# Optimization experiments

Measured on AMD Instinct MI355X. Metric: run time of the kernel, lower is better.

Reference implementation:

```python
import jax, jax.numpy as jnp
import numpy as np
from jax import lax

B, T, H, THETA_DIM = 64, 2048, 256, 5
L1, L2, OUT = 256, 256, 1


def _p(key, shape, fan_in):
    return jax.random.normal(key, shape, dtype=jnp.float32) / np.sqrt(fan_in)


def setup_inputs() -> dict:
    key = jax.random.key(0)
    ks = jax.random.split(key, 16)
    inp = {
        "x": jax.random.normal(ks[0], (B, T), dtype=jnp.float32),
        "theta": jax.random.normal(ks[1], (B, THETA_DIM), dtype=jnp.float32),
        # LSTM layer 0 (input dim 1): gate order [i, f, g, o]
        "Wx0": _p(ks[2], (1, 4 * H), 1),
        "Wh0": _p(ks[3], (H, 4 * H), H),
        "b0": jnp.zeros((4 * H,), dtype=jnp.float32),
        # LSTM layer 1 (input dim H)
        "Wx1": _p(ks[4], (H, 4 * H), H),
        "Wh1": _p(ks[5], (H, 4 * H), H),
        "b1": jnp.zeros((4 * H,), dtype=jnp.float32),
        # theta projector Dense(H)
        "Wtp": _p(ks[6], (THETA_DIM, H), THETA_DIM),
        "btp": jnp.zeros((H,), dtype=jnp.float32),
        # MLP head: concat(H + H) -> 256 -> 256 -> 1
        "Wl1": _p(ks[7], (2 * H, L1), 2 * H),
        "bl1": jnp.zeros((L1,), dtype=jnp.float32),
        "Wl2": _p(ks[8], (L1, L2), L1),
        "bl2": jnp.zeros((L2,), dtype=jnp.float32),
        "Wo": _p(ks[9], (L2, OUT), L2),
        "bo": jnp.zeros((OUT,), dtype=jnp.float32),
    }
    return inp


def _lstm_layer(x_seq, Wx, Wh, b):
    # x_seq: [B, T, D]. Precompute input-to-gate GEMM once (big, batched),
    # leaving only the small recurrent matmul inside the scan.
    xg = jnp.einsum('btd,dg->btg', x_seq, Wx) + b  # [B, T, 4H]
    bsz = x_seq.shape[0]
    h = Wh.shape[0]
    c0 = jnp.zeros((bsz, h), dtype=x_seq.dtype)
    h0 = jnp.zeros((bsz, h), dtype=x_seq.dtype)

    def step(carry, xg_t):
        c, hh = carry
        gates = xg_t + hh @ Wh  # [B, 4H]
        i, f, g, o = jnp.split(gates, 4, axis=-1)
        c = jax.nn.sigmoid(f) * c + jax.nn.sigmoid(i) * jnp.tanh(g)
        hh = jax.nn.sigmoid(o) * jnp.tanh(c)
        return (c, hh), hh

    _, hs = lax.scan(step, (c0, h0), jnp.swapaxes(xg, 0, 1))  # hs: [T, B, H]
    return jnp.swapaxes(hs, 0, 1)  # [B, T, H]


def reference(x, theta, Wx0, Wh0, b0, Wx1, Wh1, b1, Wtp, btp,
              Wl1, bl1, Wl2, bl2, Wo, bo):
    h = x[:, :, None]  # [B, T, 1] (module expands 2-D input)
    h = _lstm_layer(h, Wx0, Wh0, b0)
    h = _lstm_layer(h, Wx1, Wh1, b1)
    h = jnp.mean(h, axis=1)  # mean_aggregation=True -> [B, H]
    tproj = theta @ Wtp + btp  # [B, H]
    z = jnp.concatenate([h, tproj], axis=-1)  # [B, 2H]
    z = jax.nn.elu(z @ Wl1 + bl1)
    z = jax.nn.elu(z @ Wl2 + bl2)
    return z @ Wo + bo  # [B, 1]
```

## Files before the change

kernel.cpp:

```cpp
#include <hip/hip_runtime.h>
#include <hip/hip_bf16.h>


#define BB 64
#define TT 2048
#define HH 256

typedef short s16x8 __attribute__((ext_vector_type(8)));
typedef float f32x4 __attribute__((ext_vector_type(4)));

__device__ inline unsigned short f2bf(float f) {
  unsigned u = __float_as_uint(f);
  u += 0x7fff + ((u >> 16) & 1);
  return (unsigned short)(u >> 16);
}
__device__ inline float sigm(float x) { return 1.f / (1.f + __expf(-x)); }
__device__ inline float tanh_f(float x) { return 1.f - 2.f / (__expf(2.f * x) + 1.f); }

__device__ inline void st_wt32(unsigned int* p, unsigned int v) {
  __hip_atomic_store(p, v, __ATOMIC_RELAXED, __HIP_MEMORY_SCOPE_AGENT);
}
__device__ inline void st_flag(int* p, int v) {
  __hip_atomic_store(p, v, __ATOMIC_RELAXED, __HIP_MEMORY_SCOPE_AGENT);
}
__device__ inline unsigned long long ld_wt64(const unsigned long long* p) {
  return __hip_atomic_load(p, __ATOMIC_RELAXED, __HIP_MEMORY_SCOPE_AGENT);
}
__device__ inline void wait_ge(const int* p, int tgt) {
  while (__hip_atomic_load(p, __ATOMIC_RELAXED, __HIP_MEMORY_SCOPE_AGENT) < tgt)
    __builtin_amdgcn_s_sleep(1);
}
__device__ inline s16x8 ld_frag_wt(const unsigned short* p) {
  union { unsigned long long q[2]; s16x8 v; } u;
  u.q[0] = ld_wt64((const unsigned long long*)p);
  u.q[1] = ld_wt64((const unsigned long long*)(p + 4));
  return u.v;
}

#define MFMA(a, b, c) __builtin_amdgcn_mfma_f32_16x16x32_bf16((a), (b), (c), 0, 0, 0)

__global__ void xt_kernel(const float* __restrict__ x, float* __restrict__ xT) {
  int i = blockIdx.x * 256 + threadIdx.x;
  int b = i & 63, t = i >> 6;
  xT[(size_t)t * BB + b] = x[(size_t)b * TT + t];
}

__global__ __launch_bounds__(256, 2)
void lstm_kernel(const float* __restrict__ Wx0, const float* __restrict__ Wh0,
                 const float* __restrict__ b0v,
                 const float* __restrict__ Wx1, const float* __restrict__ Wh1,
                 const float* __restrict__ b1v,
                 const float* __restrict__ xT,
                 unsigned short* __restrict__ seq0, unsigned short* __restrict__ ring,
                 float* __restrict__ hmean, int* flags)
{
  __shared__ float gbuf[2][16][4][33];

  const int tid  = threadIdx.x;
  const int lane = tid & 63;
  const int w    = tid >> 6;
  const int u16  = lane & 15;
  const int kgrp = lane >> 4;
  const int arow = lane & 15;
  const int gp   = w & 1;

  int* f0 = flags;
  int* f1 = flags + 512;

  const int bid = blockIdx.x;

  if (bid < 32) {
    const int g = bid >> 3, wg = bid & 7;
    const int b0r = g * 16;
    const int uh = w >> 1;
    const int ubase = wg * 32;
    s16x8 bw[16];
#pragma unroll
    for (int f = 0; f < 16; ++f) {
      const int nt = f >> 3, ks = f & 7;
      const int col = (2 * gp + nt) * 256 + ubase + uh * 16 + u16;
#pragma unroll
      for (int j = 0; j < 8; ++j)
        bw[f][j] = (short)f2bf(Wh0[(size_t)(ks * 32 + kgrp * 8 + j) * 1024 + col]);
    }
    const int eur = tid >> 4;
    const int eu2 = (tid & 15) * 2;
    float bE[2][4], xE[2][4];
#pragma unroll
    for (int uu = 0; uu < 2; ++uu)
#pragma unroll
      for (int ga = 0; ga < 4; ++ga) {
        const int col = ga * 256 + ubase + eu2 + uu;
        bE[uu][ga] = b0v[col];
        xE[uu][ga] = Wx0[col];
      }
    int* myflag = &f0[(g * 8 + wg) * 16];
    float cst[2] = {0.f, 0.f};

    for (int t = 0; t < TT; ++t) {
      if (t > 0 && tid < 8) wait_ge(&f0[(g * 8 + tid) * 16], t);
      __syncthreads();

      f32x4 acc0 = {0, 0, 0, 0}, acc1 = {0, 0, 0, 0};
      if (t > 0) {
        const unsigned short* sp = seq0 + ((size_t)(t - 1) * BB + b0r + arow) * HH;
        s16x8 a[8];
#pragma unroll
        for (int ks = 0; ks < 8; ++ks) a[ks] = *(const s16x8*)(sp + ks * 32 + kgrp * 8);
#pragma unroll
        for (int ks = 0; ks < 8; ++ks) {
          acc0 = MFMA(a[ks], bw[ks], acc0);
          acc1 = MFMA(a[ks], bw[8 + ks], acc1);
        }
      }
#pragma unroll
      for (int r = 0; r < 4; ++r) {
        gbuf[0][kgrp * 4 + r][2 * gp + 0][uh * 16 + u16] = acc0[r];
        gbuf[0][kgrp * 4 + r][2 * gp + 1][uh * 16 + u16] = acc1[r];
      }
      __syncthreads();

      const float xval = xT[(size_t)t * BB + b0r + eur];
      unsigned short hb[2];
#pragma unroll
      for (int uu = 0; uu < 2; ++uu) {
        const int ul = eu2 + uu;
        const float gi = gbuf[0][eur][0][ul] + bE[uu][0] + xval * xE[uu][0];
        const float gf = gbuf[0][eur][1][ul] + bE[uu][1] + xval * xE[uu][1];
        const float gg = gbuf[0][eur][2][ul] + bE[uu][2] + xval * xE[uu][2];
        const float go = gbuf[0][eur][3][ul] + bE[uu][3] + xval * xE[uu][3];
        cst[uu] = sigm(gf) * cst[uu] + sigm(gi) * tanh_f(gg);
        const float hv = sigm(go) * tanh_f(cst[uu]);
        hb[uu] = f2bf(hv);
      }
      st_wt32((unsigned int*)(seq0 + ((size_t)t * BB + b0r + eur) * HH + ubase + eu2),
              (unsigned int)hb[0] | ((unsigned int)hb[1] << 16));
      __syncthreads();
      if (tid == 0) st_flag(myflag, t + 1);
    }
  } else {
    const int idx = bid - 32;
    const int g = idx >> 4, q = idx & 15;
    const int b0r = g * 16;
    const int kh = w >> 1;
    s16x8 bw[16];
#pragma unroll
    for (int f = 0; f < 16; ++f) {
      const int nt = f >> 3, ks = f & 7;
      const int col = (2 * gp + nt) * 256 + q * 16 + u16;
#pragma unroll
      for (int j = 0; j < 8; ++j) {
        const int k = ks * 32 + kgrp * 8 + j;
        const float wv = (kh == 0) ? Wx1[(size_t)k * 1024 + col]
                                   : Wh1[(size_t)k * 1024 + col];
        bw[f][j] = (short)f2bf(wv);
      }
    }
    const int eur = tid >> 3;
    const int eu2 = (tid & 7) * 2;
    float bE[2][4];
#pragma unroll
    for (int uu = 0; uu < 2; ++uu)
#pragma unroll
      for (int ga = 0; ga < 4; ++ga)
        bE[uu][ga] = b1v[ga * 256 + q * 16 + eu2 + uu];
    int* myflag = &f1[(g * 16 + q) * 16];
    float cst[2] = {0.f, 0.f}, hs2[2] = {0.f, 0.f};

    for (int t = 0; t < TT; ++t) {
      if (tid < 8) wait_ge(&f0[(g * 8 + tid) * 16], t + 1);
      else if (t > 0 && tid < 24) wait_ge(&f1[(g * 16 + tid - 8) * 16], t);
      __syncthreads();

      f32x4 acc0 = {0, 0, 0, 0}, acc1 = {0, 0, 0, 0};
      if (kh == 0) {
        const unsigned short* sp = seq0 + ((size_t)t * BB + b0r + arow) * HH;
        s16x8 a[8];
#pragma unroll
        for (int ks = 0; ks < 8; ++ks) a[ks] = *(const s16x8*)(sp + ks * 32 + kgrp * 8);
#pragma unroll
        for (int ks = 0; ks < 8; ++ks) {
          acc0 = MFMA(a[ks], bw[ks], acc0);
          acc1 = MFMA(a[ks], bw[8 + ks], acc1);
        }
      } else if (t > 0) {
        const unsigned short* rp = ring + ((size_t)((t - 1) & 1) * BB + b0r + arow) * HH;
        s16x8 a[8];
#pragma unroll
        for (int ks = 0; ks < 8; ++ks) a[ks] = ld_frag_wt(rp + ks * 32 + kgrp * 8);
#pragma unroll
        for (int ks = 0; ks < 8; ++ks) {
          acc0 = MFMA(a[ks], bw[ks], acc0);
          acc1 = MFMA(a[ks], bw[8 + ks], acc1);
        }
      }
#pragma unroll
      for (int r = 0; r < 4; ++r) {
        gbuf[kh][kgrp * 4 + r][2 * gp + 0][u16] = acc0[r];
        gbuf[kh][kgrp * 4 + r][2 * gp + 1][u16] = acc1[r];
      }
      __syncthreads();

      if (tid < 128) {
        unsigned short hb[2];
#pragma unroll
        for (int uu = 0; uu < 2; ++uu) {
          const int ul = eu2 + uu;
          const float gi = gbuf[0][eur][0][ul] + gbuf[1][eur][0][ul] + bE[uu][0];
          const float gf = gbuf[0][eur][1][ul] + gbuf[1][eur][1][ul] + bE[uu][1];
          const float gg = gbuf[0][eur][2][ul] + gbuf[1][eur][2][ul] + bE[uu][2];
          const float go = gbuf[0][eur][3][ul] + gbuf[1][eur][3][ul] + bE[uu][3];
          cst[uu] = sigm(gf) * cst[uu] + sigm(gi) * tanh_f(gg);
          const float hv = sigm(go) * tanh_f(cst[uu]);
          hs2[uu] += hv;
          hb[uu] = f2bf(hv);
        }
        st_wt32((unsigned int*)(ring + ((size_t)(t & 1) * BB + b0r + eur) * HH + q * 16 + eu2),
                (unsigned int)hb[0] | ((unsigned int)hb[1] << 16));
      }
      __syncthreads();
      if (tid == 0) st_flag(myflag, t + 1);
    }
    if (tid < 128) {
#pragma unroll
      for (int uu = 0; uu < 2; ++uu)
        hmean[(size_t)(b0r + eur) * HH + q * 16 + eu2 + uu] = hs2[uu] * (1.f / TT);
    }
  }
}

__global__ __launch_bounds__(256)
void mlp_kernel(const float* __restrict__ theta, const float* __restrict__ Wtp,
                const float* __restrict__ btp, const float* __restrict__ Wl1,
                const float* __restrict__ bl1, const float* __restrict__ Wl2,
                const float* __restrict__ bl2, const float* __restrict__ Wo,
                const float* __restrict__ bo, const float* __restrict__ hmean,
                float* __restrict__ out)
{
  const int b = blockIdx.x;
  const int j = threadIdx.x;
  __shared__ float z[2 * HH];
  __shared__ float z1s[HH];
  __shared__ float red[256];

  float tp = btp[j];
#pragma unroll
  for (int d = 0; d < 5; ++d) tp += theta[b * 5 + d] * Wtp[d * HH + j];
  z[j] = hmean[(size_t)b * HH + j];
  z[HH + j] = tp;
  __syncthreads();

  float a1 = bl1[j];
  for (int k = 0; k < 2 * HH; ++k) a1 += z[k] * Wl1[(size_t)k * 256 + j];
  a1 = (a1 > 0.f) ? a1 : (__expf(a1) - 1.f);
  z1s[j] = a1;
  __syncthreads();

  float a2 = bl2[j];
  for (int k = 0; k < HH; ++k) a2 += z1s[k] * Wl2[(size_t)k * 256 + j];
  a2 = (a2 > 0.f) ? a2 : (__expf(a2) - 1.f);
  red[j] = a2 * Wo[j];
  __syncthreads();
  for (int s = 128; s > 0; s >>= 1) {
    if (j < s) red[j] += red[j + s];
    __syncthreads();
  }
  if (j == 0) out[b] = red[0] + bo[0];
}

extern "C" void kernel_launch(void* const* d_in, const int* in_sizes, int n_in,
                              void* d_out, int out_size, void* d_ws, size_t ws_size,
                              hipStream_t stream) {
  const float* x    = (const float*)d_in[0];
  const float* theta= (const float*)d_in[1];
  const float* Wx0  = (const float*)d_in[2];
  const float* Wh0  = (const float*)d_in[3];
  const float* b0   = (const float*)d_in[4];
  const float* Wx1  = (const float*)d_in[5];
  const float* Wh1  = (const float*)d_in[6];
  const float* b1   = (const float*)d_in[7];
  const float* Wtp  = (const float*)d_in[8];
  const float* btp  = (const float*)d_in[9];
  const float* Wl1  = (const float*)d_in[10];
  const float* bl1  = (const float*)d_in[11];
  const float* Wl2  = (const float*)d_in[12];
  const float* bl2  = (const float*)d_in[13];
  const float* Wo   = (const float*)d_in[14];
  const float* bo   = (const float*)d_in[15];

  char* ws = (char*)d_ws;
  int* flags           = (int*)ws;
  unsigned short* ring = (unsigned short*)(ws + 8192);
  float* hmean         = (float*)(ws + 8192 + 65536);
  float* xT            = (float*)(ws + 8192 + 65536 + 65536);
  unsigned short* seq0 = (unsigned short*)(ws + 8192 + 65536 + 65536 + 524288);
  const size_t WS_NEED = 8192ull + 65536 + 65536 + 524288 + (size_t)TT * BB * HH * 2ull;
  if (ws_size < WS_NEED) return;

  hipMemsetAsync(d_ws, 0, 8192, stream);

  xt_kernel<<<dim3((BB * TT) / 256), dim3(256), 0, stream>>>(x, xT);
  lstm_kernel<<<dim3(96), dim3(256), 0, stream>>>(
      Wx0, Wh0, b0, Wx1, Wh1, b1, xT, seq0, ring, hmean, flags);
  mlp_kernel<<<dim3(BB), dim3(256), 0, stream>>>(
      theta, Wtp, btp, Wl1, bl1, Wl2, bl2, Wo, bo, hmean, (float*)d_out);
}
```

Before: 6.681 ms.

## Repartition LSTM recurrence into 32 wider 512-thread blocks with fewer inter-block flags

Reduces the persistent LSTM kernel from 96 blocks of 256 threads to 32 blocks of 512 threads. Each block now owns 64 hidden units, so each batch group synchronises with 4 peer blocks per step instead of 8 or 16. Layer-1 blocks hold both Wx1 and Wh1 fragments per thread. They stage the previous hidden state through a swizzled LDS tile using wide atomic loads, and layer-0 flags are polled lazily via a cached 'seen' value. This cuts cross-block flag traffic and per-step sync latency, at the cost of more registers per thread and serial input-then-recurrent MFMA chains within a block.

```diff
diff --git a/kernel.cpp b/kernel.cpp
--- a/kernel.cpp
+++ b/kernel.cpp
@@ -17,24 +17,21 @@
 __device__ inline float sigm(float x) { return 1.f / (1.f + __expf(-x)); }
 __device__ inline float tanh_f(float x) { return 1.f - 2.f / (__expf(2.f * x) + 1.f); }
 
-__device__ inline void st_wt32(unsigned int* p, unsigned int v) {
+__device__ inline void st32(unsigned int* p, unsigned int v) {
   __hip_atomic_store(p, v, __ATOMIC_RELAXED, __HIP_MEMORY_SCOPE_AGENT);
 }
-__device__ inline void st_flag(int* p, int v) {
+__device__ inline void st32i(int* p, int v) {
   __hip_atomic_store(p, v, __ATOMIC_RELAXED, __HIP_MEMORY_SCOPE_AGENT);
 }
-__device__ inline unsigned long long ld_wt64(const unsigned long long* p) {
+__device__ inline int ld32i(const int* p) {
   return __hip_atomic_load(p, __ATOMIC_RELAXED, __HIP_MEMORY_SCOPE_AGENT);
 }
+__device__ inline unsigned long long ld64(const unsigned int* p) {
+  return __hip_atomic_load((const unsigned long long*)p, __ATOMIC_RELAXED,
+                           __HIP_MEMORY_SCOPE_AGENT);
+}
 __device__ inline void wait_ge(const int* p, int tgt) {
-  while (__hip_atomic_load(p, __ATOMIC_RELAXED, __HIP_MEMORY_SCOPE_AGENT) < tgt)
-    __builtin_amdgcn_s_sleep(1);
-}
-__device__ inline s16x8 ld_frag_wt(const unsigned short* p) {
-  union { unsigned long long q[2]; s16x8 v; } u;
-  u.q[0] = ld_wt64((const unsigned long long*)p);
-  u.q[1] = ld_wt64((const unsigned long long*)(p + 4));
-  return u.v;
+  while (ld32i(p) < tgt) __builtin_amdgcn_s_sleep(1);
 }
 
 #define MFMA(a, b, c) __builtin_amdgcn_mfma_f32_16x16x32_bf16((a), (b), (c), 0, 0, 0)
@@ -45,16 +42,18 @@
   xT[(size_t)t * BB + b] = x[(size_t)b * TT + t];
 }
 
-__global__ __launch_bounds__(256, 2)
+__global__ __launch_bounds__(512, 1)
 void lstm_kernel(const float* __restrict__ Wx0, const float* __restrict__ Wh0,
                  const float* __restrict__ b0v,
                  const float* __restrict__ Wx1, const float* __restrict__ Wh1,
                  const float* __restrict__ b1v,
                  const float* __restrict__ xT,
-                 unsigned short* __restrict__ seq0, unsigned short* __restrict__ ring,
+                 unsigned int* __restrict__ seq0,
+                 unsigned int* __restrict__ h1ring,
                  float* __restrict__ hmean, int* flags)
 {
-  __shared__ float gbuf[2][16][4][33];
+  __shared__ float gbuf[16][4][66];
+  __shared__ __align__(16) char Ab1[8192];
 
   const int tid  = threadIdx.x;
   const int lane = tid & 63;
@@ -62,170 +61,182 @@
   const int u16  = lane & 15;
   const int kgrp = lane >> 4;
   const int arow = lane & 15;
-  const int gp   = w & 1;
+  const int bid  = blockIdx.x;
 
   int* f0 = flags;
-  int* f1 = flags + 512;
-
-  const int bid = blockIdx.x;
-
-  if (bid < 32) {
-    const int g = bid >> 3, wg = bid & 7;
-    const int b0r = g * 16;
-    const int uh = w >> 1;
-    const int ubase = wg * 32;
-    s16x8 bw[16];
-#pragma unroll
-    for (int f = 0; f < 16; ++f) {
-      const int nt = f >> 3, ks = f & 7;
-      const int col = (2 * gp + nt) * 256 + ubase + uh * 16 + u16;
-#pragma unroll
-      for (int j = 0; j < 8; ++j)
-        bw[f][j] = (short)f2bf(Wh0[(size_t)(ks * 32 + kgrp * 8 + j) * 1024 + col]);
-    }
-    const int eur = tid >> 4;
-    const int eu2 = (tid & 15) * 2;
-    float bE[2][4], xE[2][4];
-#pragma unroll
-    for (int uu = 0; uu < 2; ++uu)
-#pragma unroll
-      for (int ga = 0; ga < 4; ++ga) {
-        const int col = ga * 256 + ubase + eu2 + uu;
-        bE[uu][ga] = b0v[col];
-        xE[uu][ga] = Wx0[col];
-      }
-    int* myflag = &f0[(g * 8 + wg) * 16];
-    float cst[2] = {0.f, 0.f};
+  int* f1 = flags + 256;
+
+  const int gp = w >> 2;
+  const int uo = (w & 3) * 16;
+  const int eur = tid >> 5;
+  const int eu2 = (tid & 31) * 2;
+
+  if (bid < 16) {
+    const int g = bid >> 2, wg = bid & 3;
+    const int ub = wg * 64;
+    s16x8 bw[2][8];
+#pragma unroll
+    for (int nt = 0; nt < 2; ++nt)
+#pragma unroll
+      for (int ks = 0; ks < 8; ++ks) {
+        const int col = (2 * gp + nt) * 256 + ub + uo + u16;
+#pragma unroll
+        for (int j = 0; j < 8; ++j)
+          bw[nt][ks][j] = (short)f2bf(Wh0[(size_t)(ks * 32 + kgrp * 8 + j) * 1024 + col]);
+      }
+    float bE[4][2], xE[4][2];
+#pragma unroll
+    for (int ga = 0; ga < 4; ++ga)
+#pragma unroll
+      for (int uu = 0; uu < 2; ++uu) {
+        const int c = ga * 256 + ub + eu2 + uu;
+        bE[ga][uu] = b0v[c]; xE[ga][uu] = Wx0[c];
+      }
+    int* myf = &f0[(g * 4 + wg) * 16];
+    float cL[2] = {0.f, 0.f};
 
     for (int t = 0; t < TT; ++t) {
-      if (t > 0 && tid < 8) wait_ge(&f0[(g * 8 + tid) * 16], t);
-      __syncthreads();
-
-      f32x4 acc0 = {0, 0, 0, 0}, acc1 = {0, 0, 0, 0};
+      if (t > 0 && tid < 4) wait_ge(&f0[(g * 4 + tid) * 16], t);
+      __syncthreads();
+
+      f32x4 acc0 = {0,0,0,0}, acc1 = {0,0,0,0};
       if (t > 0) {
-        const unsigned short* sp = seq0 + ((size_t)(t - 1) * BB + b0r + arow) * HH;
+        const unsigned int* sp = seq0 + ((size_t)(t - 1) * BB + g * 16 + arow) * 128;
         s16x8 a[8];
 #pragma unroll
-        for (int ks = 0; ks < 8; ++ks) a[ks] = *(const s16x8*)(sp + ks * 32 + kgrp * 8);
+        for (int ks = 0; ks < 8; ++ks) a[ks] = *(const s16x8*)(sp + ks * 16 + kgrp * 4);
 #pragma unroll
         for (int ks = 0; ks < 8; ++ks) {
-          acc0 = MFMA(a[ks], bw[ks], acc0);
-          acc1 = MFMA(a[ks], bw[8 + ks], acc1);
+          acc0 = MFMA(a[ks], bw[0][ks], acc0);
+          acc1 = MFMA(a[ks], bw[1][ks], acc1);
         }
       }
 #pragma unroll
       for (int r = 0; r < 4; ++r) {
-        gbuf[0][kgrp * 4 + r][2 * gp + 0][uh * 16 + u16] = acc0[r];
-        gbuf[0][kgrp * 4 + r][2 * gp + 1][uh * 16 + u16] = acc1[r];
-      }
-      __syncthreads();
-
-      const float xval = xT[(size_t)t * BB + b0r + eur];
+        gbuf[kgrp * 4 + r][2 * gp + 0][uo + u16] = acc0[r];
+        gbuf[kgrp * 4 + r][2 * gp + 1][uo + u16] = acc1[r];
+      }
+      __syncthreads();
+
+      const float xval = xT[(size_t)t * BB + g * 16 + eur];
       unsigned short hb[2];
 #pragma unroll
       for (int uu = 0; uu < 2; ++uu) {
-        const int ul = eu2 + uu;
-        const float gi = gbuf[0][eur][0][ul] + bE[uu][0] + xval * xE[uu][0];
-        const float gf = gbuf[0][eur][1][ul] + bE[uu][1] + xval * xE[uu][1];
-        const float gg = gbuf[0][eur][2][ul] + bE[uu][2] + xval * xE[uu][2];
-        const float go = gbuf[0][eur][3][ul] + bE[uu][3] + xval * xE[uu][3];
-        cst[uu] = sigm(gf) * cst[uu] + sigm(gi) * tanh_f(gg);
-        const float hv = sigm(go) * tanh_f(cst[uu]);
+        const int u = eu2 + uu;
+        const float gi = gbuf[eur][0][u] + bE[0][uu] + xval * xE[0][uu];
+        const float gf = gbuf[eur][1][u] + bE[1][uu] + xval * xE[1][uu];
+        const float gg = gbuf[eur][2][u] + bE[2][uu] + xval * xE[2][uu];
+        const float go = gbuf[eur][3][u] + bE[3][uu] + xval * xE[3][uu];
+        cL[uu] = sigm(gf) * cL[uu] + sigm(gi) * tanh_f(gg);
+        const float hv = sigm(go) * tanh_f(cL[uu]);
         hb[uu] = f2bf(hv);
       }
-      st_wt32((unsigned int*)(seq0 + ((size_t)t * BB + b0r + eur) * HH + ubase + eu2),
-              (unsigned int)hb[0] | ((unsigned int)hb[1] << 16));
-      __syncthreads();
-      if (tid == 0) st_flag(myflag, t + 1);
+      st32(seq0 + ((size_t)t * BB + g * 16 + eur) * 128 + ((ub + eu2) >> 1),
+           (unsigned int)hb[0] | ((unsigned int)hb[1] << 16));
+      __syncthreads();
+      if (tid == 0) st32i(myf, t + 1);
     }
   } else {
-    const int idx = bid - 32;
-    const int g = idx >> 4, q = idx & 15;
-    const int b0r = g * 16;
-    const int kh = w >> 1;
-    s16x8 bw[16];
-#pragma unroll
-    for (int f = 0; f < 16; ++f) {
-      const int nt = f >> 3, ks = f & 7;
-      const int col = (2 * gp + nt) * 256 + q * 16 + u16;
-#pragma unroll
-      for (int j = 0; j < 8; ++j) {
-        const int k = ks * 32 + kgrp * 8 + j;
-        const float wv = (kh == 0) ? Wx1[(size_t)k * 1024 + col]
-                                   : Wh1[(size_t)k * 1024 + col];
-        bw[f][j] = (short)f2bf(wv);
-      }
+    const int idx = bid - 16, g = idx >> 2, q = idx & 3;
+    const int ub = q * 64;
+    s16x8 bw[2][16];
+#pragma unroll
+    for (int nt = 0; nt < 2; ++nt)
+#pragma unroll
+      for (int ks = 0; ks < 16; ++ks) {
+        const int col = (2 * gp + nt) * 256 + ub + uo + u16;
+#pragma unroll
+        for (int j = 0; j < 8; ++j) {
+          const int k = (ks & 7) * 32 + kgrp * 8 + j;
+          bw[nt][ks][j] = (short)f2bf((ks < 8) ? Wx1[(size_t)k * 1024 + col]
+                                               : Wh1[(size_t)k * 1024 + col]);
+        }
+      }
+    float bE[4][2];
+#pragma unroll
+    for (int ga = 0; ga < 4; ++ga)
+#pragma unroll
+      for (int uu = 0; uu < 2; ++uu)
+        bE[ga][uu] = b1v[ga * 256 + ub + eu2 + uu];
+    int* myf = &f1[(g * 4 + q) * 16];
+    unsigned int* hr = h1ring + (size_t)g * 4096;
+    const int srow = tid >> 5, sc4 = (tid & 31) * 4;
+    int seen = 0;
+    float cL[2] = {0.f, 0.f}, hs[2] = {0.f, 0.f};
+
+    for (int t = 0; t < TT; ++t) {
+      if (tid < 4) {
+        if (seen <= t) {
+          do { seen = ld32i(&f0[(g * 4 + tid) * 16]);
+               if (seen <= t) __builtin_amdgcn_s_sleep(1); } while (seen <= t);
+        }
+      } else if (t > 0 && tid < 7) {
+        int qq = tid - 4; qq += (qq >= q);
+        wait_ge(&f1[(g * 4 + qq) * 16], t);
+      }
+      __syncthreads();
+
+      unsigned long long q0 = 0, q1 = 0;
+      if (t > 0) {
+        const unsigned int* sb = hr + ((t - 1) & 1) * 2048 + srow * 128 + sc4;
+        q0 = ld64(sb); q1 = ld64(sb + 2);
+      }
+      f32x4 acc0 = {0,0,0,0}, acc1 = {0,0,0,0};
+      {
+        const unsigned int* sp = seq0 + ((size_t)t * BB + g * 16 + arow) * 128;
+        s16x8 a[8];
+#pragma unroll
+        for (int ks = 0; ks < 8; ++ks) a[ks] = *(const s16x8*)(sp + ks * 16 + kgrp * 4);
+#pragma unroll
+        for (int ks = 0; ks < 8; ++ks) {
+          acc0 = MFMA(a[ks], bw[0][ks], acc0);
+          acc1 = MFMA(a[ks], bw[1][ks], acc1);
+        }
+      }
+      if (t > 0) {
+        const unsigned int w0 = (unsigned)(q0 & 0xFFFFFFFFu), w1 = (unsigned)(q0 >> 32);
+        const unsigned int w2 = (unsigned)(q1 & 0xFFFFFFFFu), w3 = (unsigned)(q1 >> 32);
+        *(uint4*)(Ab1 + ((srow * 512 + (tid & 31) * 16) ^ ((srow & 7) << 4))) =
+            (uint4){w0, w1, w2, w3};
+        __syncthreads();
+        s16x8 a[8];
+#pragma unroll
+        for (int kk = 0; kk < 8; ++kk)
+          a[kk] = *(const s16x8*)(Ab1 + ((arow * 512 + (kk * 32 + kgrp * 8) * 2) ^ ((arow & 7) << 4)));
+#pragma unroll
+        for (int kk = 0; kk < 8; ++kk) {
+          acc0 = MFMA(a[kk], bw[0][8 + kk], acc0);
+          acc1 = MFMA(a[kk], bw[1][8 + kk], acc1);
+        }
+      }
+#pragma unroll
+      for (int r = 0; r < 4; ++r) {
+        gbuf[kgrp * 4 + r][2 * gp + 0][uo + u16] = acc0[r];
+        gbuf[kgrp * 4 + r][2 * gp + 1][uo + u16] = acc1[r];
+      }
+      __syncthreads();
+
+      unsigned short hb[2];
+#pragma unroll
+      for (int uu = 0; uu < 2; ++uu) {
+        const int u = eu2 + uu;
+        const float gi = gbuf[eur][0][u] + bE[0][uu];
+        const float gf = gbuf[eur][1][u] + bE[1][uu];
+        const float gg = gbuf[eur][2][u] + bE[2][uu];
+        const float go = gbuf[eur][3][u] + bE[3][uu];
+        cL[uu] = sigm(gf) * cL[uu] + sigm(gi) * tanh_f(gg);
+        const float hv = sigm(go) * tanh_f(cL[uu]);
+        hs[uu] += hv;
+        hb[uu] = f2bf(hv);
+      }
+      st32(hr + (t & 1) * 2048 + eur * 128 + ((ub + eu2) >> 1),
+           (unsigned int)hb[0] | ((unsigned int)hb[1] << 16));
+      __syncthreads();
+      if (tid == 0) st32i(myf, t + 1);
     }
-    const int eur = tid >> 3;
-    const int eu2 = (tid & 7) * 2;
-    float bE[2][4];
 #pragma unroll
     for (int uu = 0; uu < 2; ++uu)
-#pragma unroll
-      for (int ga = 0; ga < 4; ++ga)
-        bE[uu][ga] = b1v[ga * 256 + q * 16 + eu2 + uu];
-    int* myflag = &f1[(g * 16 + q) * 16];
-    float cst[2] = {0.f, 0.f}, hs2[2] = {0.f, 0.f};
-
-    for (int t = 0; t < TT; ++t) {
-      if (tid < 8) wait_ge(&f0[(g * 8 + tid) * 16], t + 1);
-      else if (t > 0 && tid < 24) wait_ge(&f1[(g * 16 + tid - 8) * 16], t);
-      __syncthreads();
-
-      f32x4 acc0 = {0, 0, 0, 0}, acc1 = {0, 0, 0, 0};
-      if (kh == 0) {
-        const unsigned short* sp = seq0 + ((size_t)t * BB + b0r + arow) * HH;
-        s16x8 a[8];
-#pragma unroll
-        for (int ks = 0; ks < 8; ++ks) a[ks] = *(const s16x8*)(sp + ks * 32 + kgrp * 8);
-#pragma unroll
-        for (int ks = 0; ks < 8; ++ks) {
-          acc0 = MFMA(a[ks], bw[ks], acc0);
-          acc1 = MFMA(a[ks], bw[8 + ks], acc1);
-        }
-      } else if (t > 0) {
-        const unsigned short* rp = ring + ((size_t)((t - 1) & 1) * BB + b0r + arow) * HH;
-        s16x8 a[8];
-#pragma unroll
-        for (int ks = 0; ks < 8; ++ks) a[ks] = ld_frag_wt(rp + ks * 32 + kgrp * 8);
-#pragma unroll
-        for (int ks = 0; ks < 8; ++ks) {
-          acc0 = MFMA(a[ks], bw[ks], acc0);
-          acc1 = MFMA(a[ks], bw[8 + ks], acc1);
-        }
-      }
-#pragma unroll
-      for (int r = 0; r < 4; ++r) {
-        gbuf[kh][kgrp * 4 + r][2 * gp + 0][u16] = acc0[r];
-        gbuf[kh][kgrp * 4 + r][2 * gp + 1][u16] = acc1[r];
-      }
-      __syncthreads();
-
-      if (tid < 128) {
-        unsigned short hb[2];
-#pragma unroll
-        for (int uu = 0; uu < 2; ++uu) {
-          const int ul = eu2 + uu;
-          const float gi = gbuf[0][eur][0][ul] + gbuf[1][eur][0][ul] + bE[uu][0];
-          const float gf = gbuf[0][eur][1][ul] + gbuf[1][eur][1][ul] + bE[uu][1];
-          const float gg = gbuf[0][eur][2][ul] + gbuf[1][eur][2][ul] + bE[uu][2];
-          const float go = gbuf[0][eur][3][ul] + gbuf[1][eur][3][ul] + bE[uu][3];
-          cst[uu] = sigm(gf) * cst[uu] + sigm(gi) * tanh_f(gg);
-          const float hv = sigm(go) * tanh_f(cst[uu]);
-          hs2[uu] += hv;
-          hb[uu] = f2bf(hv);
-        }
-        st_wt32((unsigned int*)(ring + ((size_t)(t & 1) * BB + b0r + eur) * HH + q * 16 + eu2),
-                (unsigned int)hb[0] | ((unsigned int)hb[1] << 16));
-      }
-      __syncthreads();
-      if (tid == 0) st_flag(myflag, t + 1);
-    }
-    if (tid < 128) {
-#pragma unroll
-      for (int uu = 0; uu < 2; ++uu)
-        hmean[(size_t)(b0r + eur) * HH + q * 16 + eu2 + uu] = hs2[uu] * (1.f / TT);
-    }
+      hmean[(size_t)(g * 16 + eur) * HH + ub + eu2 + uu] = hs[uu] * (1.f / TT);
   }
 }
 
@@ -289,19 +300,19 @@
   const float* bo   = (const float*)d_in[15];
 
   char* ws = (char*)d_ws;
-  int* flags           = (int*)ws;
-  unsigned short* ring = (unsigned short*)(ws + 8192);
-  float* hmean         = (float*)(ws + 8192 + 65536);
-  float* xT            = (float*)(ws + 8192 + 65536 + 65536);
-  unsigned short* seq0 = (unsigned short*)(ws + 8192 + 65536 + 65536 + 524288);
-  const size_t WS_NEED = 8192ull + 65536 + 65536 + 524288 + (size_t)TT * BB * HH * 2ull;
+  int* flags            = (int*)ws;
+  unsigned int* h1ring  = (unsigned int*)(ws + 8192);
+  float* hmean          = (float*)(ws + 8192 + 65536);
+  float* xT             = (float*)(ws + 8192 + 65536 + 65536);
+  unsigned int* seq0    = (unsigned int*)(ws + 8192 + 65536 + 65536 + 524288);
+  const size_t WS_NEED = 8192ull + 65536 + 65536 + 524288 + (size_t)TT * BB * 128 * 4ull;
   if (ws_size < WS_NEED) return;
 
   hipMemsetAsync(d_ws, 0, 8192, stream);
 
   xt_kernel<<<dim3((BB * TT) / 256), dim3(256), 0, stream>>>(x, xT);
-  lstm_kernel<<<dim3(96), dim3(256), 0, stream>>>(
-      Wx0, Wh0, b0, Wx1, Wh1, b1, xT, seq0, ring, hmean, flags);
+  lstm_kernel<<<dim3(32), dim3(512), 0, stream>>>(
+      Wx0, Wh0, b0, Wx1, Wh1, b1, xT, seq0, h1ring, hmean, flags);
   mlp_kernel<<<dim3(BB), dim3(256), 0, stream>>>(
       theta, Wtp, btp, Wl1, bl1, Wl2, bl2, Wo, bo, hmean, (float*)d_out);
 }
```

After: 8.394 ms. 1.26x slower.
